# Optimization experiments

Measured on AMD Instinct MI355X. Metric: run time of the kernel, lower is better.

Reference implementation:

```python
import jax, jax.numpy as jnp
import numpy as np

BL = 512              # block length (init kwarg bl)
HALF = BL // 2
WIN = BL + 2 * HALF   # window width seen by each query block
Q_DIM = K_DIM = V_DIM = 256
R1 = R2 = R3 = 2
CQ, CK, CV = Q_DIM // R1, K_DIM // R2, V_DIM // R3


def setup_inputs() -> dict:
    key = jax.random.key(0)
    ks = jax.random.split(key, 9)
    B, L = 1, 131072
    def w(k, shape, fan):
        return (jax.random.normal(k, shape, jnp.float32) / np.float32(np.sqrt(fan)))
    return {
        "x1": jax.random.normal(ks[0], (B, Q_DIM, L), jnp.float32),
        "mask": jnp.ones((B, 1, L), jnp.float32),
        "Wq": w(ks[1], (CQ, Q_DIM), Q_DIM), "bq": jnp.zeros((CQ,), jnp.float32),
        "Wk": w(ks[2], (CK, K_DIM), K_DIM), "bk": jnp.zeros((CK,), jnp.float32),
        "Wv": w(ks[3], (CV, V_DIM), V_DIM), "bv": jnp.zeros((CV,), jnp.float32),
        "Wo": w(ks[4], (V_DIM, CV), CV),   "bo": jnp.zeros((V_DIM,), jnp.float32),
    }


def conv1x1(W, b, x):
    # nn.Conv1d(kernel_size=1): (B, Cin, L) -> (B, Cout, L)
    return jnp.einsum('oc,bcl->bol', W, x) + b[None, :, None]


def _sliding_window_att(q, k, v, mask):
    B, cq, L = q.shape
    cv = v.shape[1]
    nb = L // BL  # L chosen divisible by BL (remainder-pad branch is a no-op)
    # per-frame padding mask, (B,1,L)
    pm = jnp.broadcast_to(mask[:, 0:1, :], (B, 1, L))
    # blocked queries: (B*nb, cq, BL)
    qb = q.reshape(B, cq, nb, BL).transpose(0, 2, 1, 3).reshape(B * nb, cq, BL)
    # pad k / v / mask by HALF zeros on both sides, then take overlapping windows
    kp = jnp.pad(k, ((0, 0), (0, 0), (HALF, HALF)))
    vp = jnp.pad(v, ((0, 0), (0, 0), (HALF, HALF)))
    mp = jnp.pad(pm, ((0, 0), (0, 0), (HALF, HALF)))
    idx = np.arange(nb)[:, None] * BL + np.arange(WIN)[None, :]
    kb = kp[:, :, idx].transpose(0, 2, 1, 3).reshape(B * nb, -1, WIN)
    vb = vp[:, :, idx].transpose(0, 2, 1, 3).reshape(B * nb, -1, WIN)
    mb = mp[:, :, idx].transpose(0, 2, 1, 3).reshape(B * nb, 1, WIN)
    # construct_window_mask: loop sets window_mask[:, :, i:i+BL] = 1 for i in [0,BL),
    # whose union is columns [0, 2*BL-1) for ALL rows (faithful to the given code).
    wm = (jnp.arange(WIN) < (2 * BL - 1)).astype(q.dtype)[None, None, :]
    fm = wm * mb  # final mask, broadcasts over the BL query rows
    # scalar_dot_att with log-mask trick
    energy = jnp.einsum('ncl,ncw->nlw', qb, kb) / np.float32(np.sqrt(cq))
    att = jax.nn.softmax(energy + jnp.log(fm + 1e-6), axis=-1) * fm
    out = jnp.einsum('ncw,nlw->ncl', vb, att)  # (B*nb, cv, BL)
    return out, nb, cv


def reference(x1, mask, Wq, bq, Wk, bk, Wv, bv, Wo, bo):
    B, _, L = x1.shape
    q = conv1x1(Wq, bq, x1)
    k = conv1x1(Wk, bk, x1)
    v = conv1x1(Wv, bv, x1)
    out, nb, cv = _sliding_window_att(q, k, v, mask)
    out = conv1x1(Wo, bo, jax.nn.relu(out))  # (B*nb, V_DIM, BL)
    out = out.reshape(B, nb, V_DIM, BL).transpose(0, 2, 1, 3).reshape(B, V_DIM, nb * BL)
    out = out[:, :, :L]
    return out * mask[:, 0:1, :]
```

## Files before the change

kernel.cpp:

```cpp
#include <hip/hip_runtime.h>
#include <math.h>

#define LTOT 131072

typedef unsigned short u16;
typedef unsigned int   u32;
typedef __attribute__((ext_vector_type(8))) short bf16x8;
typedef __attribute__((ext_vector_type(4))) short bf16x4;
typedef __attribute__((ext_vector_type(4))) float f32x4;

__device__ __forceinline__ u16 f2b(float f) {
  union { float f; u32 u; } v; v.f = f;
  u32 r = v.u + 0x7fffu + ((v.u >> 16) & 1u);
  return (u16)(r >> 16);
}

__device__ __forceinline__ u32 cvt_pk(float lo, float hi) {
  u32 r;
  asm("v_cvt_pk_bf16_f32 %0, %1, %2" : "=v"(r) : "v"(lo), "v"(hi));
  return r;
}

__device__ __forceinline__ bf16x8 pack_bp(const f32x4 a, const f32x4 b) {
  union { u32 w[4]; bf16x8 v; } u;
  u.w[0] = cvt_pk(a[0], a[1]);
  u.w[1] = cvt_pk(a[2], a[3]);
  u.w[2] = cvt_pk(b[0], b[1]);
  u.w[3] = cvt_pk(b[2], b[3]);
  return u.v;
}

__device__ __forceinline__ int sxt_addr(int row, int g) {
  return (row << 8) + (((g) ^ (row & 7)) << 3);
}

__global__ __launch_bounds__(512) void k_qkv(
    const float* __restrict__ x1,
    const float* __restrict__ Wq, const float* __restrict__ bq,
    const float* __restrict__ Wk, const float* __restrict__ bk,
    const float* __restrict__ Wv, const float* __restrict__ bv,
    const float* __restrict__ Wo,
    u16* __restrict__ scratch, u16* __restrict__ WoB)
{
  __shared__ __align__(16) u16 sXT[128 * 256];

  const int tid  = threadIdx.x;
  const int lane = tid & 63;
  const int wv   = tid >> 6;
  const int lr   = lane & 15;
  const int lg   = lane >> 4;
  const int l0   = blockIdx.x << 7;

  {
    const int cl = (tid & 63) << 1;
    const int kq = tid >> 6;
#pragma unroll
    for (int k8 = 0; k8 < 4; ++k8) {
      const int k0 = kq * 32 + k8 * 8;
      float2 v[8];
#pragma unroll
      for (int j = 0; j < 8; ++j)
        v[j] = *reinterpret_cast<const float2*>(x1 + (size_t)(k0 + j) * LTOT + l0 + cl);
      union { u16 h[8]; bf16x8 b; } p0, p1;
#pragma unroll
      for (int j = 0; j < 8; ++j) {
        p0.h[j] = f2b(v[j].x);
        p1.h[j] = f2b(v[j].y);
      }
      const int g = k0 >> 3;
      *reinterpret_cast<bf16x8*>(&sXT[sxt_addr(cl,     g)]) = p0.b;
      *reinterpret_cast<bf16x8*>(&sXT[sxt_addr(cl + 1, g)]) = p1.b;
    }
  }

  if (blockIdx.x == 0) {
    for (int idx = tid; idx < 32768; idx += 512) WoB[idx] = f2b(Wo[idx]);
  }
  __syncthreads();

  const float rs = 0.1275174468f;

#pragma unroll
  for (int wb = 0; wb < 2; ++wb) {
    const float* Wsel = wb ? Wk : Wq;
    const float* bsel = wb ? bk : bq;
    const int c = (wv << 4) + lr;

    bf16x8 bw[8];
    {
      const float* wrow = Wsel + (size_t)c * 256 + (lg << 3);
#pragma unroll
      for (int kc = 0; kc < 8; ++kc) {
        float4 wa = *reinterpret_cast<const float4*>(wrow + kc * 32);
        float4 wc = *reinterpret_cast<const float4*>(wrow + kc * 32 + 4);
        union { u16 h[8]; bf16x8 b; } u;
        u.h[0] = f2b(wa.x); u.h[1] = f2b(wa.y); u.h[2] = f2b(wa.z); u.h[3] = f2b(wa.w);
        u.h[4] = f2b(wc.x); u.h[5] = f2b(wc.y); u.h[6] = f2b(wc.z); u.h[7] = f2b(wc.w);
        bw[kc] = u.b;
      }
    }

    f32x4 acc[8];
#pragma unroll
    for (int mt = 0; mt < 8; ++mt) acc[mt] = (f32x4){0.f, 0.f, 0.f, 0.f};
#pragma unroll
    for (int kc = 0; kc < 8; ++kc) {
      const int g = (kc << 2) + lg;
#pragma unroll
      for (int mt = 0; mt < 8; ++mt) {
        bf16x8 a = *reinterpret_cast<const bf16x8*>(&sXT[sxt_addr((mt << 4) + lr, g)]);
        acc[mt] = __builtin_amdgcn_mfma_f32_16x16x32_bf16(a, bw[kc], acc[mt], 0, 0, 0);
      }
    }

    const float bias = bsel[c];
    const float scale = wb ? 1.f : rs;
    u16* dst = scratch + (size_t)wb * 128 * LTOT;
#pragma unroll
    for (int mt = 0; mt < 8; ++mt) {
      const int l = l0 + (mt << 4) + (lg << 2);
#pragma unroll
      for (int r = 0; r < 4; ++r)
        dst[(size_t)(l + r) * 128 + c] = f2b((acc[mt][r] + bias) * scale);
    }
  }

  {
    const int c = (wv << 4) + lr;
    bf16x8 aw[8];
    {
      const float* wrow = Wv + (size_t)c * 256 + (lg << 3);
#pragma unroll
      for (int kc = 0; kc < 8; ++kc) {
        float4 wa = *reinterpret_cast<const float4*>(wrow + kc * 32);
        float4 wc = *reinterpret_cast<const float4*>(wrow + kc * 32 + 4);
        union { u16 h[8]; bf16x8 b; } u;
        u.h[0] = f2b(wa.x); u.h[1] = f2b(wa.y); u.h[2] = f2b(wa.z); u.h[3] = f2b(wa.w);
        u.h[4] = f2b(wc.x); u.h[5] = f2b(wc.y); u.h[6] = f2b(wc.z); u.h[7] = f2b(wc.w);
        aw[kc] = u.b;
      }
    }

    f32x4 acc[8];
#pragma unroll
    for (int nt = 0; nt < 8; ++nt) acc[nt] = (f32x4){0.f, 0.f, 0.f, 0.f};
#pragma unroll
    for (int kc = 0; kc < 8; ++kc) {
      const int g = (kc << 2) + lg;
#pragma unroll
      for (int nt = 0; nt < 8; ++nt) {
        bf16x8 b = *reinterpret_cast<const bf16x8*>(&sXT[sxt_addr((nt << 4) + lr, g)]);
        acc[nt] = __builtin_amdgcn_mfma_f32_16x16x32_bf16(aw[kc], b, acc[nt], 0, 0, 0);
      }
    }

    const int c0 = (wv << 4) + (lg << 2);
    float4 bv4 = *reinterpret_cast<const float4*>(bv + c0);
    u16* dstv = scratch + (size_t)256 * LTOT;
#pragma unroll
    for (int nt = 0; nt < 8; ++nt) {
      const int p = l0 + (nt << 4) + lr;
      dstv[(size_t)(c0 + 0) * LTOT + p] = f2b(acc[nt][0] + bv4.x);
      dstv[(size_t)(c0 + 1) * LTOT + p] = f2b(acc[nt][1] + bv4.y);
      dstv[(size_t)(c0 + 2) * LTOT + p] = f2b(acc[nt][2] + bv4.z);
      dstv[(size_t)(c0 + 3) * LTOT + p] = f2b(acc[nt][3] + bv4.w);
    }
  }
}

__global__ __launch_bounds__(512, 4) void k_attn(
    const u16* __restrict__ scratch,
    const float* __restrict__ mask,
    u16* __restrict__ attT)
{
  __shared__ __align__(16) unsigned char smem[44032];
  u16*   sKT = (u16*)smem;
  u16*   sV  = (u16*)(smem + 17408);
  float* sLF = (float*)(smem + 35840);
  float* sFM = (float*)(smem + 39936);

  const int tid  = threadIdx.x;
  const int lane = tid & 63;
  const int wv   = tid >> 6;
  const int lr   = lane & 15;
  const int lg   = lane >> 4;
  const int lq0  = blockIdx.x << 7;
  const int nblk = lq0 >> 9;
  const int p_base = nblk * 512 - 256;
  const int wq0  = lq0 + wv * 16;

  const u16* QT = scratch;
  const u16* KT = scratch + (size_t)128 * LTOT;
  const u16* Vp = scratch + (size_t)256 * LTOT;

  for (int idx = tid; idx < 1024; idx += 512) {
    int p = p_base + idx;
    float fmv = 0.f;
    if (idx < 1023 && (unsigned)p < (unsigned)LTOT) fmv = mask[p];
    sFM[idx] = fmv;
    sLF[idx] = log2f(fmv + 1e-6f);
  }

  bf16x8 aQ[4];
#pragma unroll
  for (int kc = 0; kc < 4; ++kc)
    aQ[kc] = *reinterpret_cast<const bf16x8*>(
        QT + (size_t)(wq0 + lr) * 128 + kc * 32 + (lg << 3));

  float m_run = -INFINITY;
  f32x4 d4 = (f32x4){0.f, 0.f, 0.f, 0.f};
  f32x4 accO[8];
#pragma unroll
  for (int cm = 0; cm < 8; ++cm) accO[cm] = (f32x4){0.f, 0.f, 0.f, 0.f};

  uint4 rk[2], rv[2];
  {
    const int p0 = p_base;
#pragma unroll
    for (int j = 0; j < 2; ++j) {
      int idx = tid + j * 512;
      int row = idx >> 4, ch = (idx & 15) << 3;
      int p = p0 + row;
      rk[j] = make_uint4(0u, 0u, 0u, 0u);
      if ((unsigned)p < (unsigned)LTOT)
        rk[j] = *reinterpret_cast<const uint4*>(KT + (size_t)p * 128 + ch);
      int c = idx >> 3, w = (idx & 7) << 3;
      int pp = p0 + w;
      rv[j] = make_uint4(0u, 0u, 0u, 0u);
      if ((unsigned)pp < (unsigned)LTOT)
        rv[j] = *reinterpret_cast<const uint4*>(Vp + (size_t)c * LTOT + pp);
    }
  }
#pragma unroll
  for (int j = 0; j < 2; ++j) {
    int idx = tid + j * 512;
    int row = idx >> 4, ch = (idx & 15) << 3;
    *reinterpret_cast<uint4*>(&sKT[row * 136 + ch]) = rk[j];
    int c = idx >> 3, w = (idx & 7) << 3;
    *reinterpret_cast<uint4*>(&sV[c * 72 + w]) = rv[j];
  }
  __syncthreads();

  for (int it = 0; it < 16; ++it) {
    if (it < 15) {
      const int p0 = p_base + (it + 1) * 64;
#pragma unroll
      for (int j = 0; j < 2; ++j) {
        int idx = tid + j * 512;
        int row = idx >> 4, ch = (idx & 15) << 3;
        int p = p0 + row;
        rk[j] = make_uint4(0u, 0u, 0u, 0u);
        if ((unsigned)p < (unsigned)LTOT)
          rk[j] = *reinterpret_cast<const uint4*>(KT + (size_t)p * 128 + ch);
        int c = idx >> 3, w = (idx & 7) << 3;
        int pp = p0 + w;
        rv[j] = make_uint4(0u, 0u, 0u, 0u);
        if ((unsigned)pp < (unsigned)LTOT)
          rv[j] = *reinterpret_cast<const uint4*>(Vp + (size_t)c * LTOT + pp);
      }
    }

    f32x4 e[4];
#pragma unroll
    for (int nt = 0; nt < 4; ++nt) e[nt] = (f32x4){0.f, 0.f, 0.f, 0.f};
#pragma unroll
    for (int kc = 0; kc < 4; ++kc) {
      const int ko = kc * 32 + (lg << 3);
#pragma unroll
      for (int nt = 0; nt < 4; ++nt) {
        bf16x8 bk = *reinterpret_cast<const bf16x8*>(&sKT[(nt * 16 + lr) * 136 + ko]);
        e[nt] = __builtin_amdgcn_mfma_f32_16x16x32_bf16(bk, aQ[kc], e[nt], 0, 0, 0);
      }
    }

    const int wbase = it * 64 + (lg << 2);
#pragma unroll
    for (int nt = 0; nt < 4; ++nt) {
      f32x4 lf = *reinterpret_cast<const f32x4*>(&sLF[wbase + nt * 16]);
      e[nt] += lf;
    }

    float lmax = e[0][0];
#pragma unroll
    for (int nt = 0; nt < 4; ++nt)
#pragma unroll
      for (int r = 0; r < 4; ++r) if (nt || r) lmax = fmaxf(lmax, e[nt][r]);

    if (__any(lmax > m_run + 12.0f)) {
      float rmax = lmax;
      rmax = fmaxf(rmax, __shfl_xor(rmax, 16));
      rmax = fmaxf(rmax, __shfl_xor(rmax, 32));
      float mnew = fmaxf(m_run, rmax);
      float fs = exp2f(m_run - mnew);
      d4 *= fs;
#pragma unroll
      for (int cm = 0; cm < 8; ++cm) accO[cm] *= fs;
      m_run = mnew;
    }

    f32x4 pn[4];
#pragma unroll
    for (int nt = 0; nt < 4; ++nt) {
      f32x4 fmv = *reinterpret_cast<const f32x4*>(&sFM[wbase + nt * 16]);
      f32x4 pd;
#pragma unroll
      for (int r = 0; r < 4; ++r) pd[r] = exp2f(e[nt][r] - m_run);
      d4 += pd;
      pn[nt] = pd * fmv;
    }
    bf16x8 bp0 = pack_bp(pn[0], pn[1]);
    bf16x8 bp1 = pack_bp(pn[2], pn[3]);

#pragma unroll
    for (int k2 = 0; k2 < 2; ++k2) {
      const bf16x8 bp = k2 ? bp1 : bp0;
      const int vo = k2 * 32 + (lg << 2);
#pragma unroll
      for (int cm = 0; cm < 8; ++cm) {
        const u16* vr = &sV[(cm * 16 + lr) * 72 + vo];
        bf16x4 v0 = *reinterpret_cast<const bf16x4*>(vr);
        bf16x4 v1 = *reinterpret_cast<const bf16x4*>(vr + 16);
        bf16x8 av = __builtin_shufflevector(v0, v1, 0, 1, 2, 3, 4, 5, 6, 7);
        accO[cm] = __builtin_amdgcn_mfma_f32_16x16x32_bf16(av, bp, accO[cm], 0, 0, 0);
      }
    }

    __syncthreads();
    if (it < 15) {
#pragma unroll
      for (int j = 0; j < 2; ++j) {
        int idx = tid + j * 512;
        int row = idx >> 4, ch = (idx & 15) << 3;
        *reinterpret_cast<uint4*>(&sKT[row * 136 + ch]) = rk[j];
        int c = idx >> 3, w = (idx & 7) << 3;
        *reinterpret_cast<uint4*>(&sV[c * 72 + w]) = rv[j];
      }
    }
    __syncthreads();
  }

  float dsum = d4[0] + d4[1] + d4[2] + d4[3];
  dsum += __shfl_xor(dsum, 16);
  dsum += __shfl_xor(dsum, 32);
  const float rd = 1.f / dsum;

  __syncthreads();
  u16* sT = (u16*)smem + wv * 2176;
#pragma unroll
  for (int cm = 0; cm < 8; ++cm) {
    float o0 = fmaxf(accO[cm][0] * rd, 0.f);
    float o1 = fmaxf(accO[cm][1] * rd, 0.f);
    float o2 = fmaxf(accO[cm][2] * rd, 0.f);
    float o3 = fmaxf(accO[cm][3] * rd, 0.f);
    uint2 pk = make_uint2(cvt_pk(o0, o1), cvt_pk(o2, o3));
    *reinterpret_cast<uint2*>(&sT[lr * 136 + cm * 16 + (lg << 2)]) = pk;
  }
  __syncthreads();
  for (int idx = lane; idx < 256; idx += 64) {
    int row = idx >> 4, ch = (idx & 15) << 3;
    uint4 v = *reinterpret_cast<const uint4*>(&sT[row * 136 + ch]);
    *reinterpret_cast<uint4*>(attT + (size_t)(wq0 + row) * 128 + ch) = v;
  }
}

__device__ __forceinline__ int sa_addr(int row, int g) {
  return (row << 7) + (((g) ^ (row & 7)) << 3);
}

__global__ __launch_bounds__(512) void k_out(
    const u16* __restrict__ attT, const u16* __restrict__ WoB,
    const float* __restrict__ bo, const float* __restrict__ mask,
    float* __restrict__ out)
{
  __shared__ __align__(16) u16 sA[128 * 128];

  const int tid  = threadIdx.x;
  const int lane = tid & 63;
  const int wv   = tid >> 6;
  const int lr   = lane & 15;
  const int lg   = lane >> 4;
  const int l0   = blockIdx.x << 7;

  for (int idx = tid; idx < 2048; idx += 512) {
    int row = idx >> 4, g = idx & 15;
    uint4 v = *reinterpret_cast<const uint4*>(attT + (size_t)(l0 + row) * 128 + (g << 3));
    *reinterpret_cast<uint4*>(&sA[sa_addr(row, g)]) = v;
  }
  __syncthreads();

  const int ob = wv << 5;
  f32x4 acc[2][8];
#pragma unroll
  for (int mt = 0; mt < 2; ++mt)
#pragma unroll
    for (int nt = 0; nt < 8; ++nt) acc[mt][nt] = (f32x4){0.f, 0.f, 0.f, 0.f};

#pragma unroll
  for (int kc = 0; kc < 4; ++kc) {
    bf16x8 a[2], b[8];
#pragma unroll
    for (int mt = 0; mt < 2; ++mt)
      a[mt] = *reinterpret_cast<const bf16x8*>(
          WoB + (size_t)(ob + mt * 16 + lr) * 128 + kc * 32 + (lg << 3));
    const int g = (kc << 2) + lg;
#pragma unroll
    for (int nt = 0; nt < 8; ++nt)
      b[nt] = *reinterpret_cast<const bf16x8*>(&sA[sa_addr(nt * 16 + lr, g)]);
#pragma unroll
    for (int mt = 0; mt < 2; ++mt)
#pragma unroll
      for (int nt = 0; nt < 8; ++nt)
        acc[mt][nt] = __builtin_amdgcn_mfma_f32_16x16x32_bf16(a[mt], b[nt], acc[mt][nt], 0, 0, 0);
  }

#pragma unroll
  for (int mt = 0; mt < 2; ++mt) {
    const int o0 = ob + mt * 16 + (lg << 2);
    float4 b4 = *reinterpret_cast<const float4*>(bo + o0);
#pragma unroll
    for (int nt = 0; nt < 8; ++nt) {
      const int l = l0 + nt * 16 + lr;
      const float mk = mask[l];
      out[(size_t)(o0 + 0) * LTOT + l] = (acc[mt][nt][0] + b4.x) * mk;
      out[(size_t)(o0 + 1) * LTOT + l] = (acc[mt][nt][1] + b4.y) * mk;
      out[(size_t)(o0 + 2) * LTOT + l] = (acc[mt][nt][2] + b4.z) * mk;
      out[(size_t)(o0 + 3) * LTOT + l] = (acc[mt][nt][3] + b4.w) * mk;
    }
  }
}

extern "C" void kernel_launch(void* const* d_in, const int* in_sizes, int n_in,
                              void* d_out, int out_size, void* d_ws, size_t ws_size,
                              hipStream_t stream) {
  (void)in_sizes; (void)n_in; (void)out_size; (void)ws_size;
  const float* x1   = (const float*)d_in[0];
  const float* mask = (const float*)d_in[1];
  const float* Wq   = (const float*)d_in[2];
  const float* bq   = (const float*)d_in[3];
  const float* Wk   = (const float*)d_in[4];
  const float* bk   = (const float*)d_in[5];
  const float* Wv   = (const float*)d_in[6];
  const float* bv   = (const float*)d_in[7];
  const float* Wo   = (const float*)d_in[8];
  const float* bo   = (const float*)d_in[9];

  u16* scratch = (u16*)d_out;
  u16* attT    = (u16*)d_ws;
  u16* WoB     = attT + (size_t)128 * LTOT;
  float* out   = (float*)d_out;

  hipLaunchKernelGGL(k_qkv, dim3(1024), dim3(512), 0, stream,
                     x1, Wq, bq, Wk, bk, Wv, bv, Wo, scratch, WoB);
  hipLaunchKernelGGL(k_attn, dim3(1024), dim3(512), 0, stream,
                     scratch, mask, attT);
  hipLaunchKernelGGL(k_out, dim3(1024), dim3(512), 0, stream,
                     attT, WoB, bo, mask, out);
}
```

Baseline: 267.5 us.

## Swap MFMA operands for vectorized projection stores and remap attention block order

The Q/K and V projection MFMAs now take their operands in swapped order, so each lane's four accumulator values are contiguous in the output layout. The previous scattered 2-byte scalar stores become single 8-byte packed stores, which cuts the number of global store transactions. Separately, the attention kernel remaps blockIdx so that consecutive workgroups are spread across distant sequence positions, which changes the L2/cache locality pattern across XCDs. The remap could either help or hurt, since neighbouring query tiles share K/V windows.

```diff
diff --git a/kernel.cpp b/kernel.cpp
--- a/kernel.cpp
+++ b/kernel.cpp
@@ -109,19 +109,23 @@
 #pragma unroll
       for (int mt = 0; mt < 8; ++mt) {
         bf16x8 a = *reinterpret_cast<const bf16x8*>(&sXT[sxt_addr((mt << 4) + lr, g)]);
-        acc[mt] = __builtin_amdgcn_mfma_f32_16x16x32_bf16(a, bw[kc], acc[mt], 0, 0, 0);
-      }
-    }
-
-    const float bias = bsel[c];
+        acc[mt] = __builtin_amdgcn_mfma_f32_16x16x32_bf16(bw[kc], a, acc[mt], 0, 0, 0);
+      }
+    }
+
+    const int c0 = (wv << 4) + (lg << 2);
+    float4 b4 = *reinterpret_cast<const float4*>(bsel + c0);
+    const float bb[4] = {b4.x, b4.y, b4.z, b4.w};
     const float scale = wb ? 1.f : rs;
     u16* dst = scratch + (size_t)wb * 128 * LTOT;
 #pragma unroll
     for (int mt = 0; mt < 8; ++mt) {
-      const int l = l0 + (mt << 4) + (lg << 2);
+      const int l = l0 + (mt << 4) + lr;
+      union { u16 h[4]; uint2 v; } s;
 #pragma unroll
       for (int r = 0; r < 4; ++r)
-        dst[(size_t)(l + r) * 128 + c] = f2b((acc[mt][r] + bias) * scale);
+        s.h[r] = f2b((acc[mt][r] + bb[r]) * scale);
+      *reinterpret_cast<uint2*>(dst + (size_t)l * 128 + c0) = s.v;
     }
   }
 
@@ -150,20 +154,20 @@
 #pragma unroll
       for (int nt = 0; nt < 8; ++nt) {
         bf16x8 b = *reinterpret_cast<const bf16x8*>(&sXT[sxt_addr((nt << 4) + lr, g)]);
-        acc[nt] = __builtin_amdgcn_mfma_f32_16x16x32_bf16(aw[kc], b, acc[nt], 0, 0, 0);
-      }
-    }
-
-    const int c0 = (wv << 4) + (lg << 2);
-    float4 bv4 = *reinterpret_cast<const float4*>(bv + c0);
-    u16* dstv = scratch + (size_t)256 * LTOT;
+        acc[nt] = __builtin_amdgcn_mfma_f32_16x16x32_bf16(b, aw[kc], acc[nt], 0, 0, 0);
+      }
+    }
+
+    const float bias = bv[c];
+    u16* dstv = scratch + (size_t)256 * LTOT + (size_t)c * LTOT;
 #pragma unroll
     for (int nt = 0; nt < 8; ++nt) {
-      const int p = l0 + (nt << 4) + lr;
-      dstv[(size_t)(c0 + 0) * LTOT + p] = f2b(acc[nt][0] + bv4.x);
-      dstv[(size_t)(c0 + 1) * LTOT + p] = f2b(acc[nt][1] + bv4.y);
-      dstv[(size_t)(c0 + 2) * LTOT + p] = f2b(acc[nt][2] + bv4.z);
-      dstv[(size_t)(c0 + 3) * LTOT + p] = f2b(acc[nt][3] + bv4.w);
+      const int p0 = l0 + (nt << 4) + (lg << 2);
+      union { u16 h[4]; uint2 v; } s;
+#pragma unroll
+      for (int r = 0; r < 4; ++r)
+        s.h[r] = f2b(acc[nt][r] + bias);
+      *reinterpret_cast<uint2*>(dstv + p0) = s.v;
     }
   }
 }
@@ -184,7 +188,8 @@
   const int wv   = tid >> 6;
   const int lr   = lane & 15;
   const int lg   = lane >> 4;
-  const int lq0  = blockIdx.x << 7;
+  const int lid  = ((int)blockIdx.x & 7) * 128 + ((int)blockIdx.x >> 3);
+  const int lq0  = lid << 7;
   const int nblk = lq0 >> 9;
   const int p_base = nblk * 512 - 256;
   const int wq0  = lq0 + wv * 16;
```

New measurement: 250.6 us. 6.3% less time.
